# Kernel tuning notes

Measured on AMD Instinct MI355X. Metric: run time of the kernel, lower is better.

The kernel has to match this reference:

```python
import jax, jax.numpy as jnp
import numpy as np

NUM_BRANCHES = 4
REP_DIM = 1024
FEAT_DIM = 128
N_DATA = 100000
NCE_K = 4096
NCE_T = 0.07
BATCH = 128
EPS = 1e-07


def setup_inputs() -> dict:
    key = jax.random.key(0)
    ks = jax.random.split(key, 8)
    d = {}
    for i in range(NUM_BRANCHES):
        d[f"emb{i}"] = jax.random.normal(ks[i], (BATCH, REP_DIM), dtype=jnp.float32)
    d["W"] = jax.random.normal(ks[4], (NUM_BRANCHES, FEAT_DIM, REP_DIM), dtype=jnp.float32) * 0.03
    d["b"] = jnp.zeros((NUM_BRANCHES, FEAT_DIM), dtype=jnp.float32)
    stdv = 1.0 / np.sqrt(FEAT_DIM / 3.0)
    d["memory"] = jax.random.uniform(ks[5], (NUM_BRANCHES, N_DATA, FEAT_DIM), dtype=jnp.float32, minval=-stdv, maxval=stdv)
    idx = jax.random.randint(ks[6], (BATCH,), 0, N_DATA)
    neg = jax.random.randint(ks[7], (BATCH, NCE_K), 0, N_DATA)
    d["idx"] = idx
    d["contrast_idx"] = jnp.concatenate([idx[:, None], neg], axis=1)  # col 0 = positive
    return d


def reference(emb0, emb1, emb2, emb3, W, b, memory, idx, contrast_idx):
    # per-branch Embed: flatten -> Linear -> L2 normalize
    embs = jnp.stack([emb0, emb1, emb2, emb3], axis=0)            # [R,B,rep]
    h = jnp.einsum('rbi,rdi->rbd', embs, W) + b[:, None, :]        # [R,B,D]
    e = h / jnp.sqrt(jnp.sum(h * h, axis=-1, keepdims=True))       # Normalize(power=2)

    # ContrastMemory: gather K+1 bank rows per sample per branch (detached)
    w = jax.lax.stop_gradient(memory[:, contrast_idx, :])          # [R,B,K+1,D]
    # scores[i,j,b,k] = <bank_j row, emb_i>  for every ordered pair
    scores = jnp.einsum('jbkd,ibd->ijbk', w, e)                    # [R,R,B,K+1]
    out = jnp.exp(scores / NCE_T)
    Z = jax.lax.stop_gradient(jnp.mean(out, axis=(2, 3)) * N_DATA)  # per-pair Z estimate
    out = out / Z[:, :, None, None]

    # ContrastLoss (Eq 11)
    m = float(NCE_K)
    Pn = 1.0 / float(N_DATA)
    pos = out[:, :, :, 0]                                          # [R,R,B]
    neg = out[:, :, :, 1:]                                         # [R,R,B,K]
    log_D1 = jnp.log(pos / (pos + m * Pn + EPS))
    log_D0 = jnp.log((m * Pn) / (neg + m * Pn + EPS))
    per_pair = -(jnp.sum(log_D1, axis=2) + jnp.sum(log_D0, axis=(2, 3))) / BATCH
    mask = 1.0 - jnp.eye(NUM_BRANCHES, dtype=per_pair.dtype)       # only i != j pairs
    return jnp.sum(per_pair * mask)
```

## Files before the change

kernel.cpp:

```cpp
#include <hip/hip_runtime.h>
#include <math.h>

#define NBR    4
#define REP    1024
#define FD     128
#define NDATA  100000
#define KP1    4097
#define BN     128
#define MPN    0.04096f
#define EPS_C  1e-7f
#define TINV   (1.0f / 0.07f)
#define NSLOT  64
#define TREFS  (BN * KP1)

typedef _Float16 half2e  __attribute__((ext_vector_type(2)));
typedef float    floatx4 __attribute__((ext_vector_type(4)));

static __device__ __forceinline__ unsigned short f2h(float f) {
    union { _Float16 h; unsigned short u; } c; c.h = (_Float16)f; return c.u;
}
static __device__ __forceinline__ float h_lo(unsigned int u) {
    union { unsigned int u; _Float16 h[2]; } c; c.u = u; return (float)c.h[0];
}
static __device__ __forceinline__ float h_hi(unsigned int u) {
    union { unsigned int u; _Float16 h[2]; } c; c.u = u; return (float)c.h[1];
}
static __device__ __forceinline__ half2e u2h2(unsigned int u) {
    union { unsigned int u; half2e h; } c; c.u = u; return c.h;
}
static __device__ __forceinline__ unsigned short f2bf(float f) {
    union { float f; unsigned int u; } c; c.f = f;
    unsigned int u = c.u;
    u += 0x7fffu + ((u >> 16) & 1u);
    return (unsigned short)(u >> 16);
}
static __device__ __forceinline__ float bf2f(unsigned short h) {
    union { unsigned int u; float f; } c; c.u = ((unsigned int)h) << 16;
    return c.f;
}

__global__ void k_init2(int* __restrict__ cnts, float* __restrict__ Zsl,
                        float* __restrict__ out) {
    const int i = blockIdx.x * 256 + threadIdx.x;
    if (i < 200004) cnts[i] = 0;
    if (i < NSLOT * 16) Zsl[i] = 0.f;
    if (i == 0) out[0] = 0.f;
}

__global__ __launch_bounds__(256)
void k_fh(const float* __restrict__ e0, const float* __restrict__ e1,
          const float* __restrict__ e2, const float* __restrict__ e3,
          const float* __restrict__ W, const float* __restrict__ bias,
          const int* __restrict__ cidx,
          ushort* __restrict__ eh2, int* __restrict__ counts) {
    const int tid = threadIdx.x;
    if ((int)blockIdx.x < NBR * BN) {
        __shared__ float s_emb[REP];
        __shared__ float s_part[256];
        __shared__ float s_sq[FD];
        const int u = blockIdx.x;
        const int r = u >> 7;
        const int b = u & 127;
        const float* emb = (r == 0 ? e0 : r == 1 ? e1 : r == 2 ? e2 : e3)
                           + (size_t)b * REP;
        for (int t = tid; t < REP; t += 256) s_emb[t] = emb[t];
        __syncthreads();
        const int d  = tid & 127;
        const int kh = tid >> 7;
        const float4* wrow = (const float4*)(W + ((size_t)r * FD + d) * REP)
                             + kh * 128;
        const float* se = s_emb + (kh << 9);
        float a = 0.f;
#pragma unroll 4
        for (int c = 0; c < 128; ++c) {
            float4 v = wrow[c];
            a += v.x * se[4*c+0] + v.y * se[4*c+1]
               + v.z * se[4*c+2] + v.w * se[4*c+3];
        }
        s_part[tid] = a;
        __syncthreads();
        float h = 0.f;
        if (kh == 0) {
            h = s_part[d] + s_part[128 + d] + bias[r * FD + d];
            s_sq[d] = h * h;
        }
        __syncthreads();
        for (int off = 64; off > 0; off >>= 1) {
            if (tid < off) s_sq[tid] += s_sq[tid + off];
            __syncthreads();
        }
        float nrm = sqrtf(s_sq[0]);
        if (kh == 0) {
            eh2[((size_t)(b * 16 + (d >> 3)) * 4 + r) * 8 + (d & 7)]
                = f2h(h / nrm);
        }
    } else {
        const int NT = 256 * 256;
        for (int t = ((int)blockIdx.x - NBR * BN) * 256 + tid; t < TREFS; t += NT)
            atomicAdd(&counts[cidx[t]], 1);
    }
}

__global__ void k_assign(const int* __restrict__ counts, int* __restrict__ start,
                         int* __restrict__ cursor) {
    __shared__ int s[256];
    __shared__ int sbase;
    const int tid = threadIdx.x;
    const int n = blockIdx.x * 256 + tid;
    int c = (n < NDATA) ? counts[n] : 0;
    s[tid] = c;
    __syncthreads();
#pragma unroll
    for (int off = 1; off < 256; off <<= 1) {
        int v = (tid >= off) ? s[tid - off] : 0;
        __syncthreads();
        s[tid] += v;
        __syncthreads();
    }
    if (tid == 255) sbase = atomicAdd(cursor, s[255]);
    __syncthreads();
    if (n < NDATA) start[n] = sbase + s[tid] - c;
}

__global__ void k_scatter(const int* __restrict__ cidx, const int* __restrict__ start,
                          int* __restrict__ fill, unsigned long long* __restrict__ inv64,
                          int* __restrict__ posc) {
    const int k = blockIdx.x * 256 + threadIdx.x;
    if (k >= KP1) return;
    const int b = blockIdx.y;
    const int n = cidx[(size_t)b * KP1 + k];
    const int pos = atomicAdd(&fill[n], 1);
    const int c = start[n] + pos;
    inv64[c] =
        ((unsigned long long)(unsigned int)n << 20) |
        ((unsigned long long)(unsigned int)b << 13) |
        (unsigned long long)(unsigned int)k;
    if (k == 0) posc[b] = c;
}

__global__ __launch_bounds__(256)
void k_pass1i(const float* __restrict__ mem, const ushort* __restrict__ eh2,
              const unsigned long long* __restrict__ inv64,
              float* __restrict__ Zsl, ushort* __restrict__ expS) {
    const int tid  = threadIdx.x;
    const int lane = tid & 63;
    const int wv   = tid >> 6;
    const int g    = ((int)blockIdx.x << 2) + wv;
    const int l4   = lane & 15;
    const int jj   = lane >> 4;
    const bool f3  = (l4 & 8) != 0;
    const bool fl2 = (l4 & 4) != 0;

    const int base = g * 64 + (g < 128 ? g : 128);
    const int end  = base + 64 + (g < 128 ? 1 : 0);

    const float* mrow = mem + (size_t)jj * (NDATA * FD) + l4 * 8;
    const uint4* e4   = (const uint4*)eh2;

    float z = 0.f;

    half2e mh0 = half2e{(_Float16)0.f, (_Float16)0.f};
    half2e mh1 = mh0, mh2 = mh0, mh3 = mh0;
    floatx4 pr0, pr1;
    int cur_n = -1;

    unsigned long long v0 = inv64[base];
    unsigned long long v1 = inv64[base + 1];
    unsigned long long v2 = (base + 2 < end) ? inv64[base + 2] : v1;
    unsigned long long v3 = (base + 3 < end) ? inv64[base + 3] : v2;

    uint4 qA0, qA1, qA2, qA3, qB0, qB1, qB2, qB3;
    {
        const uint4* p = e4 + ((size_t)(((unsigned)v0 & 0xFFFFFu) >> 13) * 16 + l4) * 4;
        qA0 = p[0]; qA1 = p[1]; qA2 = p[2]; qA3 = p[3];
    }
    {
        const uint4* p = e4 + ((size_t)(((unsigned)v1 & 0xFFFFFu) >> 13) * 16 + l4) * 4;
        qB0 = p[0]; qB1 = p[1]; qB2 = p[2]; qB3 = p[3];
    }

    int pend_n = (int)(v0 >> 20);
    {
        const floatx4* mp = (const floatx4*)(mrow + (size_t)pend_n * FD);
        pr0 = __builtin_nontemporal_load(mp);
        pr1 = __builtin_nontemporal_load(mp + 1);
    }

    auto cvt = [&]() {
        mh0 = half2e{(_Float16)pr0.x, (_Float16)pr0.y};
        mh1 = half2e{(_Float16)pr0.z, (_Float16)pr0.w};
        mh2 = half2e{(_Float16)pr1.x, (_Float16)pr1.y};
        mh3 = half2e{(_Float16)pr1.z, (_Float16)pr1.w};
    };
    auto ldrow = [&](int n) {
        const floatx4* mp = (const floatx4*)(mrow + (size_t)n * FD);
        pr0 = __builtin_nontemporal_load(mp);
        pr1 = __builtin_nontemporal_load(mp + 1);
        pend_n = n;
    };
    auto proc = [&](int cc, const uint4& q0, const uint4& q1,
                    const uint4& q2, const uint4& q3) {
        float a0 = 0.f, a1 = 0.f, a2 = 0.f, a3 = 0.f;
        a0 = __builtin_amdgcn_fdot2(mh0, u2h2(q0.x), a0, false);
        a0 = __builtin_amdgcn_fdot2(mh1, u2h2(q0.y), a0, false);
        a0 = __builtin_amdgcn_fdot2(mh2, u2h2(q0.z), a0, false);
        a0 = __builtin_amdgcn_fdot2(mh3, u2h2(q0.w), a0, false);
        a1 = __builtin_amdgcn_fdot2(mh0, u2h2(q1.x), a1, false);
        a1 = __builtin_amdgcn_fdot2(mh1, u2h2(q1.y), a1, false);
        a1 = __builtin_amdgcn_fdot2(mh2, u2h2(q1.z), a1, false);
        a1 = __builtin_amdgcn_fdot2(mh3, u2h2(q1.w), a1, false);
        a2 = __builtin_amdgcn_fdot2(mh0, u2h2(q2.x), a2, false);
        a2 = __builtin_amdgcn_fdot2(mh1, u2h2(q2.y), a2, false);
        a2 = __builtin_amdgcn_fdot2(mh2, u2h2(q2.z), a2, false);
        a2 = __builtin_amdgcn_fdot2(mh3, u2h2(q2.w), a2, false);
        a3 = __builtin_amdgcn_fdot2(mh0, u2h2(q3.x), a3, false);
        a3 = __builtin_amdgcn_fdot2(mh1, u2h2(q3.y), a3, false);
        a3 = __builtin_amdgcn_fdot2(mh2, u2h2(q3.z), a3, false);
        a3 = __builtin_amdgcn_fdot2(mh3, u2h2(q3.w), a3, false);
        float t0 = __shfl_xor(f3 ? a0 : a2, 8, 64);
        float t1 = __shfl_xor(f3 ? a1 : a3, 8, 64);
        float c0 = (f3 ? a2 : a0) + t0;
        float c1 = (f3 ? a3 : a1) + t1;
        float t2 = __shfl_xor(fl2 ? c0 : c1, 4, 64);
        float dd = (fl2 ? c1 : c0) + t2;
        dd += __shfl_xor(dd, 2, 64);
        dd += __shfl_xor(dd, 1, 64);
        float x = __expf(dd * TINV);
        z += x;
        if ((lane & 3) == 0)
            expS[(size_t)cc * 16 + (lane >> 2)] = f2h(x);
    };

    int c = base;
    for (; c + 1 < end; c += 2) {
        const int n0 = (int)(v0 >> 20);
        if (n0 != cur_n) {
            if (n0 != pend_n) ldrow(n0);
            cvt();
            cur_n = n0;
        }
        const int n1 = (int)(v1 >> 20);
        if (n1 != cur_n && n1 != pend_n) ldrow(n1);
        proc(c, qA0, qA1, qA2, qA3);
        {
            const uint4* p = e4 + ((size_t)(((unsigned)v2 & 0xFFFFFu) >> 13) * 16 + l4) * 4;
            qA0 = p[0]; qA1 = p[1]; qA2 = p[2]; qA3 = p[3];
        }
        if (n1 != cur_n) { cvt(); cur_n = n1; }
        const int n2 = (int)(v2 >> 20);
        if (n2 != cur_n && n2 != pend_n) ldrow(n2);
        proc(c + 1, qB0, qB1, qB2, qB3);
        {
            const uint4* p = e4 + ((size_t)(((unsigned)v3 & 0xFFFFFu) >> 13) * 16 + l4) * 4;
            qB0 = p[0]; qB1 = p[1]; qB2 = p[2]; qB3 = p[3];
        }
        v0 = v2; v1 = v3;
        v2 = (c + 4 < end) ? inv64[c + 4] : v3;
        v3 = (c + 5 < end) ? inv64[c + 5] : v2;
    }
    if (c < end) {
        const int n0 = (int)(v0 >> 20);
        if (n0 != cur_n) {
            if (n0 != pend_n) ldrow(n0);
            cvt();
            cur_n = n0;
        }
        proc(c, qA0, qA1, qA2, qA3);
    }

    __shared__ float s_z[4][16];
    const int i = ((l4 >> 3) << 1) | ((l4 >> 2) & 1);
    if ((lane & 3) == 0) s_z[wv][i * 4 + jj] = z;
    __syncthreads();
    if (tid < 16) {
        float vv = s_z[0][tid] + s_z[1][tid] + s_z[2][tid] + s_z[3][tid];
        const int slot = blockIdx.x & (NSLOT - 1);
        atomicAdd(&Zsl[slot * 16 + tid], vv);
    }
}

__global__ __launch_bounds__(256)
void k_pass2s(const uint4* __restrict__ esu, const float* __restrict__ Zsl,
              const int* __restrict__ posc, float* __restrict__ out) {
    const int tid = threadIdx.x;
    __shared__ float s_zinv[16];
    if (tid < 16) {
        const int comp = ((tid & 3) << 2) | (tid >> 2);
        float s = 0.f;
        for (int sl = 0; sl < NSLOT; ++sl) s += Zsl[sl * 16 + comp];
        float Z = s * (float)((double)NDATA / ((double)BN * (double)KP1));
        s_zinv[tid] = 1.0f / Z;
    }
    __syncthreads();

    float acc[16];
#pragma unroll
    for (int t = 0; t < 16; ++t) acc[t] = 0.f;

    const int NT = gridDim.x * 256;
    for (int t = blockIdx.x * 256 + tid; t < TREFS; t += NT) {
        uint4 p0 = esu[(size_t)t * 2];
        uint4 p1 = esu[(size_t)t * 2 + 1];
        unsigned int wds[8] = {p0.x, p0.y, p0.z, p0.w, p1.x, p1.y, p1.z, p1.w};
#pragma unroll
        for (int w = 0; w < 8; ++w) {
            float v0 = h_lo(wds[w]) * s_zinv[2*w];
            float v1 = h_hi(wds[w]) * s_zinv[2*w+1];
            acc[2*w]   += -__logf(1.f + (v0 + EPS_C) * (1.f / MPN));
            acc[2*w+1] += -__logf(1.f + (v1 + EPS_C) * (1.f / MPN));
        }
    }

#pragma unroll
    for (int t = 0; t < 16; ++t) {
#pragma unroll
        for (int off = 32; off > 0; off >>= 1)
            acc[t] += __shfl_down(acc[t], off, 64);
    }
    __shared__ float s_a[4][16];
    const int wv = tid >> 6;
    if ((tid & 63) == 0) {
#pragma unroll
        for (int t = 0; t < 16; ++t) s_a[wv][t] = acc[t];
    }
    __syncthreads();
    if (tid < 16) {
        float v = s_a[0][tid] + s_a[1][tid] + s_a[2][tid] + s_a[3][tid];
        v = ((tid >> 2) != (tid & 3)) ? v : 0.f;
        v += __shfl_down(v, 8, 64);
        v += __shfl_down(v, 4, 64);
        v += __shfl_down(v, 2, 64);
        v += __shfl_down(v, 1, 64);
        if (tid == 0) atomicAdd(out, -v / (float)BN);
    }

    if (blockIdx.x == 0) {
        float corr = 0.f;
        if (tid < BN) {
            const int cc = posc[tid];
            uint4 p0 = esu[(size_t)cc * 2];
            uint4 p1 = esu[(size_t)cc * 2 + 1];
            unsigned int wds[8] = {p0.x, p0.y, p0.z, p0.w, p1.x, p1.y, p1.z, p1.w};
#pragma unroll
            for (int w = 0; w < 8; ++w) {
#pragma unroll
                for (int hl = 0; hl < 2; ++hl) {
                    const int h = 2 * w + hl;
                    if ((h >> 2) != (h & 3)) {
                        float val = hl ? h_hi(wds[w]) : h_lo(wds[w]);
                        float v = val * s_zinv[h];
                        float posT = -__logf(1.f + (MPN + EPS_C) / v);
                        float negT = -__logf(1.f + (v + EPS_C) * (1.f / MPN));
                        corr += posT - negT;
                    }
                }
            }
        }
        for (int off = 32; off > 0; off >>= 1)
            corr += __shfl_down(corr, off, 64);
        __shared__ float s_c[4];
        if ((tid & 63) == 0) s_c[wv] = corr;
        __syncthreads();
        if (tid == 0)
            atomicAdd(out, -(s_c[0] + s_c[1] + s_c[2] + s_c[3]) / (float)BN);
    }
}

__global__ void k_feat(const float* __restrict__ e0, const float* __restrict__ e1,
                       const float* __restrict__ e2, const float* __restrict__ e3,
                       const float* __restrict__ W, const float* __restrict__ bias,
                       float* __restrict__ e_out) {
    const int r = blockIdx.x;
    const int b = blockIdx.y;
    const float* emb = (r == 0 ? e0 : r == 1 ? e1 : r == 2 ? e2 : e3) + (size_t)b * REP;

    __shared__ float s_emb[REP];
    for (int i = threadIdx.x; i < REP; i += blockDim.x) s_emb[i] = emb[i];
    __syncthreads();

    const int d = threadIdx.x;
    const float4* wrow = (const float4*)(W + ((size_t)r * FD + d) * REP);
    float acc = 0.f;
#pragma unroll 8
    for (int c = 0; c < REP / 4; ++c) {
        float4 v = wrow[c];
        acc += v.x * s_emb[4*c+0] + v.y * s_emb[4*c+1]
             + v.z * s_emb[4*c+2] + v.w * s_emb[4*c+3];
    }
    float h = acc + bias[r * FD + d];

    __shared__ float red[FD];
    red[d] = h * h;
    __syncthreads();
    for (int off = FD / 2; off > 0; off >>= 1) {
        if (d < off) red[d] += red[d + off];
        __syncthreads();
    }
    float nrm = sqrtf(red[0]);
    e_out[((size_t)r * BN + b) * FD + d] = h / nrm;
}

static __device__ __forceinline__ void dot4(const float4* __restrict__ row,
                                            const float* __restrict__ se,
                                            float& a0, float& a1, float& a2, float& a3) {
    a0 = a1 = a2 = a3 = 0.f;
#pragma unroll 8
    for (int c = 0; c < FD / 4; ++c) {
        float4 v = row[c];
        const int o = 4 * c;
        a0 += v.x * se[0*FD+o+0] + v.y * se[0*FD+o+1] + v.z * se[0*FD+o+2] + v.w * se[0*FD+o+3];
        a1 += v.x * se[1*FD+o+0] + v.y * se[1*FD+o+1] + v.z * se[1*FD+o+2] + v.w * se[1*FD+o+3];
        a2 += v.x * se[2*FD+o+0] + v.y * se[2*FD+o+1] + v.z * se[2*FD+o+2] + v.w * se[2*FD+o+3];
        a3 += v.x * se[3*FD+o+0] + v.y * se[3*FD+o+1] + v.z * se[3*FD+o+2] + v.w * se[3*FD+o+3];
    }
}

static __device__ __forceinline__ void block_reduce4(float z0, float z1, float z2,
                                                     float z3, float* dst, int j) {
    __shared__ float sred[256];
    float zs[NBR] = {z0, z1, z2, z3};
    for (int i = 0; i < NBR; ++i) {
        sred[threadIdx.x] = zs[i];
        __syncthreads();
        for (int off = 128; off > 0; off >>= 1) {
            if ((int)threadIdx.x < off) sred[threadIdx.x] += sred[threadIdx.x + off];
            __syncthreads();
        }
        if (threadIdx.x == 0) atomicAdd(&dst[i * NBR + j], sred[0]);
        __syncthreads();
    }
}

static __device__ __forceinline__ float term_of(float ex, float zinv, int k) {
    const float c = MPN + EPS_C;
    float v = ex * zinv;
    if (k == 0) return -__logf(1.0f + c / v);
    return -__logf(1.0f + (v + EPS_C) * (1.0f / MPN));
}

template <bool STORE>
__global__ void k_pass1_f32(const float* __restrict__ e, const float* __restrict__ memory,
                            const int* __restrict__ cidx,
                            float* __restrict__ Zsum, ushort4* __restrict__ expS) {
    const int j = blockIdx.z;
    const int b = blockIdx.y;

    __shared__ float s_e[NBR * FD];
    for (int t = threadIdx.x; t < NBR * FD; t += blockDim.x) {
        int i = t >> 7, d = t & (FD - 1);
        s_e[t] = e[((size_t)i * BN + b) * FD + d];
    }
    __syncthreads();

    const int* ci = cidx + (size_t)b * KP1;
    const float4* mem4 = (const float4*)(memory + (size_t)j * NDATA * FD);
    float z0 = 0.f, z1 = 0.f, z2 = 0.f, z3 = 0.f;

    for (int k = threadIdx.x + blockIdx.x * blockDim.x; k < KP1;
         k += blockDim.x * gridDim.x) {
        const int n = ci[k];
        const float4* row = mem4 + (size_t)n * (FD / 4);
        float a0, a1, a2, a3;
        dot4(row, s_e, a0, a1, a2, a3);
        float x0 = __expf(a0 * TINV);
        float x1 = __expf(a1 * TINV);
        float x2 = __expf(a2 * TINV);
        float x3 = __expf(a3 * TINV);
        z0 += x0; z1 += x1; z2 += x2; z3 += x3;
        if (STORE) {
            ushort4 st;
            st.x = f2bf(x0); st.y = f2bf(x1); st.z = f2bf(x2); st.w = f2bf(x3);
            expS[((size_t)j * BN + b) * KP1 + k] = st;
        }
    }
    block_reduce4(z0, z1, z2, z3, Zsum, j);
}

__global__ void k_pass2_stored(const ushort4* __restrict__ expS,
                               const float* __restrict__ Zsum,
                               float* __restrict__ accum) {
    const int j = blockIdx.z;
    const int b = blockIdx.y;

    __shared__ float s_zinv[NBR];
    if (threadIdx.x < NBR) {
        float Z = Zsum[threadIdx.x * NBR + j] *
                  (float)((double)NDATA / ((double)BN * (double)KP1));
        s_zinv[threadIdx.x] = 1.0f / Z;
    }
    __syncthreads();

    const ushort4* es = expS + ((size_t)j * BN + b) * KP1;
    float a0 = 0.f, a1 = 0.f, a2 = 0.f, a3 = 0.f;

    for (int k = threadIdx.x + blockIdx.x * blockDim.x; k < KP1;
         k += blockDim.x * gridDim.x) {
        ushort4 v = es[k];
        a0 += term_of(bf2f(v.x), s_zinv[0], k);
        a1 += term_of(bf2f(v.y), s_zinv[1], k);
        a2 += term_of(bf2f(v.z), s_zinv[2], k);
        a3 += term_of(bf2f(v.w), s_zinv[3], k);
    }
    block_reduce4(a0, a1, a2, a3, accum, j);
}

__global__ void k_pass2_regather(const float* __restrict__ e, const float* __restrict__ memory,
                                 const int* __restrict__ cidx,
                                 const float* __restrict__ Zsum, float* __restrict__ accum) {
    const int j = blockIdx.z;
    const int b = blockIdx.y;

    __shared__ float s_e[NBR * FD];
    __shared__ float s_zinv[NBR];
    for (int t = threadIdx.x; t < NBR * FD; t += blockDim.x) {
        int i = t >> 7, d = t & (FD - 1);
        s_e[t] = e[((size_t)i * BN + b) * FD + d];
    }
    if (threadIdx.x < NBR) {
        float Z = Zsum[threadIdx.x * NBR + j] *
                  (float)((double)NDATA / ((double)BN * (double)KP1));
        s_zinv[threadIdx.x] = 1.0f / Z;
    }
    __syncthreads();

    const int* ci = cidx + (size_t)b * KP1;
    const float4* mem4 = (const float4*)(memory + (size_t)j * NDATA * FD);
    float a0s = 0.f, a1s = 0.f, a2s = 0.f, a3s = 0.f;

    for (int k = threadIdx.x + blockIdx.x * blockDim.x; k < KP1;
         k += blockDim.x * gridDim.x) {
        const int n = ci[k];
        const float4* row = mem4 + (size_t)n * (FD / 4);
        float a0, a1, a2, a3;
        dot4(row, s_e, a0, a1, a2, a3);
        a0s += term_of(__expf(a0 * TINV), s_zinv[0], k);
        a1s += term_of(__expf(a1 * TINV), s_zinv[1], k);
        a2s += term_of(__expf(a2 * TINV), s_zinv[2], k);
        a3s += term_of(__expf(a3 * TINV), s_zinv[3], k);
    }
    block_reduce4(a0s, a1s, a2s, a3s, accum, j);
}

__global__ void k_init(float* __restrict__ p, int n) {
    int i = blockIdx.x * blockDim.x + threadIdx.x;
    if (i < n) p[i] = 0.f;
}

__global__ void k_final_legacy(const float* __restrict__ accum, float* __restrict__ out) {
    if (threadIdx.x == 0) {
        float s = 0.f;
        for (int i = 0; i < NBR; ++i)
            for (int j = 0; j < NBR; ++j)
                if (i != j) s += -accum[i * NBR + j] / (float)BN;
        out[0] = s;
    }
}

extern "C" void kernel_launch(void* const* d_in, const int* in_sizes, int n_in,
                              void* d_out, int out_size, void* d_ws, size_t ws_size,
                              hipStream_t stream) {
    const float* e0   = (const float*)d_in[0];
    const float* e1   = (const float*)d_in[1];
    const float* e2   = (const float*)d_in[2];
    const float* e3   = (const float*)d_in[3];
    const float* W    = (const float*)d_in[4];
    const float* bias = (const float*)d_in[5];
    const float* mem  = (const float*)d_in[6];
    const int*   cidx = (const int*)d_in[8];
    float* out = (float*)d_out;

    float* ws    = (float*)d_ws;
    float* e     = ws;
    float* Zsum  = ws + 65536;
    float* accum = ws + 65552;
    float* Zsl   = ws + 65568;
    const size_t base_b  = (size_t)67616 * 4;
    const size_t cnt_b   = (size_t)NDATA * 4;
    const size_t inv_b   = (size_t)TREFS * 8;
    const size_t expS_b  = (size_t)TREFS * 16 * 2;
    const size_t eh2_b   = (size_t)BN * 16 * 4 * 8 * 2;

    const size_t off_counts = base_b;
    const size_t off_fill   = off_counts + cnt_b;
    const size_t off_cursor = off_fill + cnt_b;
    const size_t off_start  = off_cursor + 16;
    const size_t off_inv    = off_start + cnt_b;
    const size_t off_expS   = off_inv + inv_b;
    const size_t off_eh2    = off_expS + expS_b;
    const size_t off_posc   = off_eh2 + eh2_b;

    const size_t need_main = off_posc + 512;
    const size_t need_mid  = base_b + expS_b;

    if (ws_size >= need_main) {
        int* counts  = (int*)((char*)d_ws + off_counts);
        int* fill    = (int*)((char*)d_ws + off_fill);
        int* cursor  = (int*)((char*)d_ws + off_cursor);
        int* start   = (int*)((char*)d_ws + off_start);
        unsigned long long* inv64 = (unsigned long long*)((char*)d_ws + off_inv);
        ushort* expS = (ushort*)((char*)d_ws + off_expS);
        ushort* eh2  = (ushort*)((char*)d_ws + off_eh2);
        int* posc    = (int*)((char*)d_ws + off_posc);

        k_init2<<<782, 256, 0, stream>>>(counts, Zsl, out);
        k_fh<<<NBR * BN + 256, 256, 0, stream>>>(e0, e1, e2, e3, W, bias, cidx,
                                                 eh2, counts);
        k_assign<<<391, 256, 0, stream>>>(counts, start, cursor);
        k_scatter<<<dim3(17, BN), 256, 0, stream>>>(cidx, start, fill, inv64, posc);
        k_pass1i<<<2048, 256, 0, stream>>>(mem, eh2, inv64, Zsl, expS);
        k_pass2s<<<1024, 256, 0, stream>>>((const uint4*)expS, Zsl, posc, out);
    } else {
        k_init<<<9, 256, 0, stream>>>(Zsum, 2080);
        k_feat<<<dim3(NBR, BN), 128, 0, stream>>>(e0, e1, e2, e3, W, bias, e);
        if (ws_size >= need_mid) {
            ushort4* expS = (ushort4*)((char*)d_ws + base_b);
            k_pass1_f32<true><<<dim3(4, BN, NBR), 256, 0, stream>>>(e, mem, cidx, Zsum, expS);
            k_pass2_stored<<<dim3(4, BN, NBR), 256, 0, stream>>>(expS, Zsum, accum);
        } else {
            k_pass1_f32<false><<<dim3(4, BN, NBR), 256, 0, stream>>>(e, mem, cidx, Zsum, nullptr);
            k_pass2_regather<<<dim3(4, BN, NBR), 256, 0, stream>>>(e, mem, cidx, Zsum, accum);
        }
        k_final_legacy<<<1, 64, 0, stream>>>(accum, out);
    }
}
```

Measured before the change: 525.4 us.

## Stage fp16 embeddings in LDS with a swizzle for a 1024-thread pass1 kernel

```diff
diff --git a/kernel.cpp b/kernel.cpp
--- a/kernel.cpp
+++ b/kernel.cpp
@@ -138,6 +138,118 @@
     if (k == 0) posc[b] = c;
 }
 
+__global__ __launch_bounds__(1024)
+void k_pass1L(const float* __restrict__ mem, const ushort* __restrict__ eh2g,
+              const unsigned long long* __restrict__ inv64,
+              float* __restrict__ Zsl, ushort* __restrict__ expS) {
+    extern __shared__ char smem[];
+    const int tid  = threadIdx.x;
+    const int lane = tid & 63;
+    const int wv   = tid >> 6;
+    const int l4   = lane & 15;
+    const int jj   = lane >> 4;
+    const bool f3  = (l4 & 8) != 0;
+    const bool fl2 = (l4 & 4) != 0;
+
+    {
+        const uint4* src = (const uint4*)eh2g;
+        uint4* dst = (uint4*)smem;
+        for (int ch = tid; ch < 8192; ch += 1024) {
+            const int q   = ch & 3;
+            const int cl4 = (ch >> 2) & 15;
+            const int cb  = ch >> 6;
+            const int s   = (q + ((cl4 >> 1) & 3)) & 3;
+            dst[cb * 64 + cl4 * 4 + s] = src[ch];
+        }
+    }
+    __syncthreads();
+
+    const int l4h = (l4 >> 1) & 3;
+    const int o0 = (l4 * 4 + ((0 + l4h) & 3)) * 16;
+    const int o1 = (l4 * 4 + ((1 + l4h) & 3)) * 16;
+    const int o2 = (l4 * 4 + ((2 + l4h) & 3)) * 16;
+    const int o3 = (l4 * 4 + ((3 + l4h) & 3)) * 16;
+
+    const int g    = (int)blockIdx.x * 16 + wv;
+    const int base = g * 128 + (g < 128 ? g : 128);
+    const int end  = base + 128 + (g < 128 ? 1 : 0);
+
+    const float* mrow = mem + (size_t)jj * (NDATA * FD) + l4 * 8;
+    ushort* esp = expS + (size_t)base * 16 + (lane >> 2);
+
+    float z = 0.f;
+    int n_prev = -1;
+    half2e mh0 = half2e{(_Float16)0.f, (_Float16)0.f};
+    half2e mh1 = mh0, mh2 = mh0, mh3 = mh0;
+
+    unsigned long long vnext = inv64[base];
+    for (int c = base; c < end; ++c, esp += 16) {
+        const unsigned long long v = vnext;
+        if (c + 1 < end) vnext = inv64[c + 1];
+        const int n = (int)(v >> 20);
+        const int b = (int)(((unsigned)v >> 13) & 127u);
+
+        const char* eb = smem + (b << 10);
+        uint4 ev0 = *(const uint4*)(eb + o0);
+        uint4 ev1 = *(const uint4*)(eb + o1);
+        uint4 ev2 = *(const uint4*)(eb + o2);
+        uint4 ev3 = *(const uint4*)(eb + o3);
+
+        if (n != n_prev) {
+            const floatx4* mp = (const floatx4*)(mrow + (size_t)n * FD);
+            floatx4 r0 = __builtin_nontemporal_load(mp);
+            floatx4 r1 = __builtin_nontemporal_load(mp + 1);
+            mh0 = half2e{(_Float16)r0.x, (_Float16)r0.y};
+            mh1 = half2e{(_Float16)r0.z, (_Float16)r0.w};
+            mh2 = half2e{(_Float16)r1.x, (_Float16)r1.y};
+            mh3 = half2e{(_Float16)r1.z, (_Float16)r1.w};
+            n_prev = n;
+        }
+
+        float a0 = 0.f, a1 = 0.f, a2 = 0.f, a3 = 0.f;
+        a0 = __builtin_amdgcn_fdot2(mh0, u2h2(ev0.x), a0, false);
+        a0 = __builtin_amdgcn_fdot2(mh1, u2h2(ev0.y), a0, false);
+        a0 = __builtin_amdgcn_fdot2(mh2, u2h2(ev0.z), a0, false);
+        a0 = __builtin_amdgcn_fdot2(mh3, u2h2(ev0.w), a0, false);
+        a1 = __builtin_amdgcn_fdot2(mh0, u2h2(ev1.x), a1, false);
+        a1 = __builtin_amdgcn_fdot2(mh1, u2h2(ev1.y), a1, false);
+        a1 = __builtin_amdgcn_fdot2(mh2, u2h2(ev1.z), a1, false);
+        a1 = __builtin_amdgcn_fdot2(mh3, u2h2(ev1.w), a1, false);
+        a2 = __builtin_amdgcn_fdot2(mh0, u2h2(ev2.x), a2, false);
+        a2 = __builtin_amdgcn_fdot2(mh1, u2h2(ev2.y), a2, false);
+        a2 = __builtin_amdgcn_fdot2(mh2, u2h2(ev2.z), a2, false);
+        a2 = __builtin_amdgcn_fdot2(mh3, u2h2(ev2.w), a2, false);
+        a3 = __builtin_amdgcn_fdot2(mh0, u2h2(ev3.x), a3, false);
+        a3 = __builtin_amdgcn_fdot2(mh1, u2h2(ev3.y), a3, false);
+        a3 = __builtin_amdgcn_fdot2(mh2, u2h2(ev3.z), a3, false);
+        a3 = __builtin_amdgcn_fdot2(mh3, u2h2(ev3.w), a3, false);
+
+        float t0 = __shfl_xor(f3 ? a0 : a2, 8, 64);
+        float t1 = __shfl_xor(f3 ? a1 : a3, 8, 64);
+        float c0 = (f3 ? a2 : a0) + t0;
+        float c1 = (f3 ? a3 : a1) + t1;
+        float t2 = __shfl_xor(fl2 ? c0 : c1, 4, 64);
+        float dd = (fl2 ? c1 : c0) + t2;
+        dd += __shfl_xor(dd, 2, 64);
+        dd += __shfl_xor(dd, 1, 64);
+        float x = __expf(dd * TINV);
+        z += x;
+        if ((lane & 3) == 0) *esp = f2h(x);
+    }
+
+    __shared__ float s_z[16][16];
+    const int i = ((l4 >> 3) << 1) | ((l4 >> 2) & 1);
+    if ((lane & 3) == 0) s_z[wv][i * 4 + jj] = z;
+    __syncthreads();
+    if (tid < 16) {
+        float vv = 0.f;
+#pragma unroll
+        for (int w = 0; w < 16; ++w) vv += s_z[w][tid];
+        const int slot = blockIdx.x & (NSLOT - 1);
+        atomicAdd(&Zsl[slot * 16 + tid], vv);
+    }
+}
+
 __global__ __launch_bounds__(256)
 void k_pass1i(const float* __restrict__ mem, const ushort* __restrict__ eh2,
               const unsigned long long* __restrict__ inv64,
@@ -158,65 +270,49 @@
     const uint4* e4   = (const uint4*)eh2;
 
     float z = 0.f;
-
+    int n_prev = -1;
     half2e mh0 = half2e{(_Float16)0.f, (_Float16)0.f};
     half2e mh1 = mh0, mh2 = mh0, mh3 = mh0;
-    floatx4 pr0, pr1;
-    int cur_n = -1;
-
-    unsigned long long v0 = inv64[base];
-    unsigned long long v1 = inv64[base + 1];
-    unsigned long long v2 = (base + 2 < end) ? inv64[base + 2] : v1;
-    unsigned long long v3 = (base + 3 < end) ? inv64[base + 3] : v2;
-
-    uint4 qA0, qA1, qA2, qA3, qB0, qB1, qB2, qB3;
-    {
-        const uint4* p = e4 + ((size_t)(((unsigned)v0 & 0xFFFFFu) >> 13) * 16 + l4) * 4;
-        qA0 = p[0]; qA1 = p[1]; qA2 = p[2]; qA3 = p[3];
-    }
-    {
-        const uint4* p = e4 + ((size_t)(((unsigned)v1 & 0xFFFFFu) >> 13) * 16 + l4) * 4;
-        qB0 = p[0]; qB1 = p[1]; qB2 = p[2]; qB3 = p[3];
-    }
-
-    int pend_n = (int)(v0 >> 20);
-    {
-        const floatx4* mp = (const floatx4*)(mrow + (size_t)pend_n * FD);
-        pr0 = __builtin_nontemporal_load(mp);
-        pr1 = __builtin_nontemporal_load(mp + 1);
-    }
-
-    auto cvt = [&]() {
-        mh0 = half2e{(_Float16)pr0.x, (_Float16)pr0.y};
-        mh1 = half2e{(_Float16)pr0.z, (_Float16)pr0.w};
-        mh2 = half2e{(_Float16)pr1.x, (_Float16)pr1.y};
-        mh3 = half2e{(_Float16)pr1.z, (_Float16)pr1.w};
-    };
-    auto ldrow = [&](int n) {
-        const floatx4* mp = (const floatx4*)(mrow + (size_t)n * FD);
-        pr0 = __builtin_nontemporal_load(mp);
-        pr1 = __builtin_nontemporal_load(mp + 1);
-        pend_n = n;
-    };
-    auto proc = [&](int cc, const uint4& q0, const uint4& q1,
-                    const uint4& q2, const uint4& q3) {
+
+    unsigned long long vnext = inv64[base];
+    for (int c = base; c < end; ++c) {
+        const unsigned long long v = vnext;
+        if (c + 1 < end) vnext = inv64[c + 1];
+        const int n = (int)(v >> 20);
+        const int b = (int)(((unsigned)v >> 13) & 127u);
+
+        const uint4* p = e4 + ((size_t)b * 16 + l4) * 4;
+        uint4 ev0 = p[0], ev1 = p[1], ev2 = p[2], ev3 = p[3];
+
+        if (n != n_prev) {
+            const floatx4* mp = (const floatx4*)(mrow + (size_t)n * FD);
+            floatx4 r0 = __builtin_nontemporal_load(mp);
+            floatx4 r1 = __builtin_nontemporal_load(mp + 1);
+            mh0 = half2e{(_Float16)r0.x, (_Float16)r0.y};
+            mh1 = half2e{(_Float16)r0.z, (_Float16)r0.w};
+            mh2 = half2e{(_Float16)r1.x, (_Float16)r1.y};
+            mh3 = half2e{(_Float16)r1.z, (_Float16)r1.w};
+            n_prev = n;
+        }
+
         float a0 = 0.f, a1 = 0.f, a2 = 0.f, a3 = 0.f;
-        a0 = __builtin_amdgcn_fdot2(mh0, u2h2(q0.x), a0, false);
-        a0 = __builtin_amdgcn_fdot2(mh1, u2h2(q0.y), a0, false);
-        a0 = __builtin_amdgcn_fdot2(mh2, u2h2(q0.z), a0, false);
-        a0 = __builtin_amdgcn_fdot2(mh3, u2h2(q0.w), a0, false);
-        a1 = __builtin_amdgcn_fdot2(mh0, u2h2(q1.x), a1, false);
-        a1 = __builtin_amdgcn_fdot2(mh1, u2h2(q1.y), a1, false);
-        a1 = __builtin_amdgcn_fdot2(mh2, u2h2(q1.z), a1, false);
-        a1 = __builtin_amdgcn_fdot2(mh3, u2h2(q1.w), a1, false);
-        a2 = __builtin_amdgcn_fdot2(mh0, u2h2(q2.x), a2, false);
-        a2 = __builtin_amdgcn_fdot2(mh1, u2h2(q2.y), a2, false);
-        a2 = __builtin_amdgcn_fdot2(mh2, u2h2(q2.z), a2, false);
-        a2 = __builtin_amdgcn_fdot2(mh3, u2h2(q2.w), a2, false);
-        a3 = __builtin_amdgcn_fdot2(mh0, u2h2(q3.x), a3, false);
-        a3 = __builtin_amdgcn_fdot2(mh1, u2h2(q3.y), a3, false);
-        a3 = __builtin_amdgcn_fdot2(mh2, u2h2(q3.z), a3, false);
-        a3 = __builtin_amdgcn_fdot2(mh3, u2h2(q3.w), a3, false);
+        a0 = __builtin_amdgcn_fdot2(mh0, u2h2(ev0.x), a0, false);
+        a0 = __builtin_amdgcn_fdot2(mh1, u2h2(ev0.y), a0, false);
+        a0 = __builtin_amdgcn_fdot2(mh2, u2h2(ev0.z), a0, false);
+        a0 = __builtin_amdgcn_fdot2(mh3, u2h2(ev0.w), a0, false);
+        a1 = __builtin_amdgcn_fdot2(mh0, u2h2(ev1.x), a1, false);
+        a1 = __builtin_amdgcn_fdot2(mh1, u2h2(ev1.y), a1, false);
+        a1 = __builtin_amdgcn_fdot2(mh2, u2h2(ev1.z), a1, false);
+        a1 = __builtin_amdgcn_fdot2(mh3, u2h2(ev1.w), a1, false);
+        a2 = __builtin_amdgcn_fdot2(mh0, u2h2(ev2.x), a2, false);
+        a2 = __builtin_amdgcn_fdot2(mh1, u2h2(ev2.y), a2, false);
+        a2 = __builtin_amdgcn_fdot2(mh2, u2h2(ev2.z), a2, false);
+        a2 = __builtin_amdgcn_fdot2(mh3, u2h2(ev2.w), a2, false);
+        a3 = __builtin_amdgcn_fdot2(mh0, u2h2(ev3.x), a3, false);
+        a3 = __builtin_amdgcn_fdot2(mh1, u2h2(ev3.y), a3, false);
+        a3 = __builtin_amdgcn_fdot2(mh2, u2h2(ev3.z), a3, false);
+        a3 = __builtin_amdgcn_fdot2(mh3, u2h2(ev3.w), a3, false);
+
         float t0 = __shfl_xor(f3 ? a0 : a2, 8, 64);
         float t1 = __shfl_xor(f3 ? a1 : a3, 8, 64);
         float c0 = (f3 ? a2 : a0) + t0;
@@ -228,44 +324,7 @@
         float x = __expf(dd * TINV);
         z += x;
         if ((lane & 3) == 0)
-            expS[(size_t)cc * 16 + (lane >> 2)] = f2h(x);
-    };
-
-    int c = base;
-    for (; c + 1 < end; c += 2) {
-        const int n0 = (int)(v0 >> 20);
-        if (n0 != cur_n) {
-            if (n0 != pend_n) ldrow(n0);
-            cvt();
-            cur_n = n0;
-        }
-        const int n1 = (int)(v1 >> 20);
-        if (n1 != cur_n && n1 != pend_n) ldrow(n1);
-        proc(c, qA0, qA1, qA2, qA3);
-        {
-            const uint4* p = e4 + ((size_t)(((unsigned)v2 & 0xFFFFFu) >> 13) * 16 + l4) * 4;
-            qA0 = p[0]; qA1 = p[1]; qA2 = p[2]; qA3 = p[3];
-        }
-        if (n1 != cur_n) { cvt(); cur_n = n1; }
-        const int n2 = (int)(v2 >> 20);
-        if (n2 != cur_n && n2 != pend_n) ldrow(n2);
-        proc(c + 1, qB0, qB1, qB2, qB3);
-        {
-            const uint4* p = e4 + ((size_t)(((unsigned)v3 & 0xFFFFFu) >> 13) * 16 + l4) * 4;
-            qB0 = p[0]; qB1 = p[1]; qB2 = p[2]; qB3 = p[3];
-        }
-        v0 = v2; v1 = v3;
-        v2 = (c + 4 < end) ? inv64[c + 4] : v3;
-        v3 = (c + 5 < end) ? inv64[c + 5] : v2;
-    }
-    if (c < end) {
-        const int n0 = (int)(v0 >> 20);
-        if (n0 != cur_n) {
-            if (n0 != pend_n) ldrow(n0);
-            cvt();
-            cur_n = n0;
-        }
-        proc(c, qA0, qA1, qA2, qA3);
+            expS[(size_t)c * 16 + (lane >> 2)] = f2h(x);
     }
 
     __shared__ float s_z[4][16];
@@ -607,7 +666,11 @@
                                                  eh2, counts);
         k_assign<<<391, 256, 0, stream>>>(counts, start, cursor);
         k_scatter<<<dim3(17, BN), 256, 0, stream>>>(cidx, start, fill, inv64, posc);
-        k_pass1i<<<2048, 256, 0, stream>>>(mem, eh2, inv64, Zsl, expS);
+        (void)hipGetLastError();
+        k_pass1L<<<256, 1024, 131072, stream>>>(mem, eh2, inv64, Zsl, expS);
+        if (hipGetLastError() != hipSuccess) {
+            k_pass1i<<<2048, 256, 0, stream>>>(mem, eh2, inv64, Zsl, expS);
+        }
         k_pass2s<<<1024, 256, 0, stream>>>((const uint4*)expS, Zsl, posc, out);
     } else {
         k_init<<<9, 256, 0, stream>>>(Zsum, 2080);
```

Result: faster. 471.2 us (-10.3%).
